# Kernel optimization log

Measured on AMD Instinct MI355X. Metric: run time of the kernel, lower is better.

The kernel has to match this reference:

```python
import jax, jax.numpy as jnp
import numpy as np


def setup_inputs() -> dict:
    key = jax.random.key(0)
    ks = jax.random.split(key, 6)
    B, S, H, F, E = 4, 2048, 1024, 4096, 8
    x = jax.random.normal(ks[0], (B, S, H), dtype=jnp.float32)
    Wr = jax.random.normal(ks[1], (H, E), dtype=jnp.float32) * (1.0 / np.sqrt(H))
    br = jnp.zeros((E,), dtype=jnp.float32)
    W1 = jax.random.normal(ks[2], (E, H, F), dtype=jnp.float32) * (1.0 / np.sqrt(H))
    b1 = jnp.zeros((E, F), dtype=jnp.float32)
    W2 = jax.random.normal(ks[3], (E, F, H), dtype=jnp.float32) * (1.0 / np.sqrt(F))
    b2 = jnp.zeros((E, H), dtype=jnp.float32)
    b_buf = jnp.zeros((E,), dtype=jnp.float32)  # load-balancing bias buffer, zero-init
    return {"x": x, "b_buf": b_buf, "Wr": Wr, "br": br,
            "W1": W1, "b1": b1, "W2": W2, "b2": b2, "k": 2}


def reference(x, b_buf, Wr, br, W1, b1, W2, b2, k):
    # Router
    scores = jnp.einsum('bsh,he->bse', x, Wr) + br          # [B,S,E]
    probs = jax.nn.softmax(scores, axis=-1)
    # load_balancing: expert selection uses biased scores (b_buf pre-update)
    _, expert_id = jax.lax.top_k(probs + b_buf, k)          # [B,S,k] int
    # combine weights use unbiased probs
    p, _ = jax.lax.top_k(probs, k)                          # [B,S,k]
    # Dense-dispatch reference: run every expert MLP on all tokens,
    # then select via one-hot mask (same math as gather/scatter dispatch).
    h1 = jnp.einsum('bsh,ehf->ebsf', x, W1) + b1[:, None, None, :]
    h1 = jax.nn.gelu(h1, approximate=False)                 # torch nn.GELU = exact
    out_e = jnp.einsum('ebsf,efh->ebsh', h1, W2) + b2[:, None, None, :]
    E = W1.shape[0]
    onehot = (expert_id[None, :, :, :] == jnp.arange(E)[:, None, None, None]).astype(x.dtype)  # [E,B,S,k]
    out_k = jnp.einsum('ebsk,ebsh->bskh', onehot, out_e)    # scatter-combine per slot
    w = p / jnp.sum(p, axis=-1, keepdims=True)              # normalize top-k probs
    return jnp.einsum('bsk,bskh->bsh', w, out_k)
```

## Files before the change

### kernel.cpp

```cpp
#include <hip/hip_runtime.h>
#include <stdint.h>

#define NTOK 8192
#define H_ 1024
#define F_ 4096
#define E_ 8
#define ROWS_CAP 17408
#define MBLK 136

using f32x4  = __attribute__((ext_vector_type(4))) float;
using short8 = __attribute__((ext_vector_type(8))) short;

__device__ __forceinline__ ushort f2bf(float f) {
  union { float f; uint32_t u; } v; v.f = f;
  uint32_t r = (v.u + 0x7FFFu + ((v.u >> 16) & 1u)) >> 16;
  return (ushort)r;
}

__global__ void k_init(int* cnt, int* cur, int* tok, float* wl) {
  int i = blockIdx.x * 256 + threadIdx.x;
  if (i < E_) { cnt[i] = 0; cur[i] = 0; }
  if (i < ROWS_CAP) { tok[i] = -1; wl[i] = 0.f; }
}

__global__ __launch_bounds__(256) void k_transcvt(const float* __restrict__ W,
                                                  ushort* __restrict__ WT,
                                                  int R, int C) {
  __shared__ float t[64][65];
  int e = blockIdx.z;
  int c0 = blockIdx.x * 64, r0 = blockIdx.y * 64;
  const float* Wp = W + (size_t)e * R * C;
  ushort* Tp = WT + (size_t)e * R * C;
  int tx = threadIdx.x & 15, ty = threadIdx.x >> 4;
#pragma unroll
  for (int i = 0; i < 4; i++) {
    int lr = ty + i * 16;
    const float4 v = *(const float4*)&Wp[(size_t)(r0 + lr) * C + c0 + tx * 4];
    t[lr][tx * 4 + 0] = v.x; t[lr][tx * 4 + 1] = v.y;
    t[lr][tx * 4 + 2] = v.z; t[lr][tx * 4 + 3] = v.w;
  }
  __syncthreads();
#pragma unroll
  for (int i = 0; i < 4; i++) {
    int lc = ty + i * 16;
    ushort4 o;
    o.x = f2bf(t[tx * 4 + 0][lc]);
    o.y = f2bf(t[tx * 4 + 1][lc]);
    o.z = f2bf(t[tx * 4 + 2][lc]);
    o.w = f2bf(t[tx * 4 + 3][lc]);
    *(ushort4*)&Tp[(size_t)(c0 + lc) * R + r0 + tx * 4] = o;
  }
}

__global__ __launch_bounds__(256) void k_router(const float* __restrict__ x,
                                                const float* __restrict__ Wr,
                                                const float* __restrict__ br,
                                                const float* __restrict__ bbuf,
                                                int* cnt, int* te, float* tw) {
  int wid = threadIdx.x >> 6, lane = threadIdx.x & 63;
  int t = blockIdx.x * 4 + wid;
  const float* xp = x + (size_t)t * H_;
  double acc[E_];
#pragma unroll
  for (int e = 0; e < E_; e++) acc[e] = 0.0;
  for (int j = lane; j < H_; j += 64) {
    float xv = xp[j];
    const float4 w0 = *(const float4*)&Wr[j * 8];
    const float4 w1 = *(const float4*)&Wr[j * 8 + 4];
    acc[0] += (double)xv * (double)w0.x;
    acc[1] += (double)xv * (double)w0.y;
    acc[2] += (double)xv * (double)w0.z;
    acc[3] += (double)xv * (double)w0.w;
    acc[4] += (double)xv * (double)w1.x;
    acc[5] += (double)xv * (double)w1.y;
    acc[6] += (double)xv * (double)w1.z;
    acc[7] += (double)xv * (double)w1.w;
  }
#pragma unroll
  for (int e = 0; e < E_; e++)
    for (int s = 32; s > 0; s >>= 1) acc[e] += __shfl_xor(acc[e], s);
  if (lane == 0) {
    double s[E_], m = -1e300;
    for (int e = 0; e < E_; e++) { s[e] = acc[e] + (double)br[e]; if (s[e] > m) m = s[e]; }
    double pe[E_], sum = 0.0;
    for (int e = 0; e < E_; e++) { pe[e] = exp(s[e] - m); sum += pe[e]; }
    double pr[E_], bb[E_];
    for (int e = 0; e < E_; e++) { pr[e] = pe[e] / sum; bb[e] = pr[e] + (double)bbuf[e]; }
    int e0 = 0;
    for (int e = 1; e < E_; e++) if (bb[e] > bb[e0]) e0 = e;
    int e1 = (e0 == 0) ? 1 : 0;
    for (int e = 0; e < E_; e++) if (e != e0 && bb[e] > bb[e1]) e1 = e;
    int a0 = 0;
    for (int e = 1; e < E_; e++) if (pr[e] > pr[a0]) a0 = e;
    int a1 = (a0 == 0) ? 1 : 0;
    for (int e = 0; e < E_; e++) if (e != a0 && pr[e] > pr[a1]) a1 = e;
    double iv = 1.0 / (pr[a0] + pr[a1]);
    te[t * 2] = e0; te[t * 2 + 1] = e1;
    tw[t * 2] = (float)(pr[a0] * iv); tw[t * 2 + 1] = (float)(pr[a1] * iv);
    atomicAdd(&cnt[e0], 1); atomicAdd(&cnt[e1], 1);
  }
}

__global__ void k_offsets(const int* cnt, int* off) {
  if (threadIdx.x == 0 && blockIdx.x == 0) {
    int o = 0; off[0] = 0;
    for (int e = 0; e < E_; e++) { o += ((cnt[e] + 127) >> 7) << 7; off[e + 1] = o; }
  }
}

__global__ void k_build(const int* __restrict__ te, const float* __restrict__ tw,
                        const int* __restrict__ off, int* cur, int* tok, float* wl) {
  int t = blockIdx.x * 256 + threadIdx.x;
  if (t >= NTOK) return;
#pragma unroll
  for (int s = 0; s < 2; s++) {
    int e = te[t * 2 + s];
    int slot = atomicAdd(&cur[e], 1);
    int pos = off[e] + slot;
    tok[pos] = t; wl[pos] = tw[t * 2 + s];
  }
}

__global__ __launch_bounds__(256) void k_gather(const float* __restrict__ x,
                                                const int* __restrict__ tok,
                                                ushort* __restrict__ Xg) {
  int row = blockIdx.x;
  int t = tok[row];
  if (t < 0) return;
  const float4* src = (const float4*)(x + (size_t)t * H_);
  ushort4* dst = (ushort4*)(Xg + (size_t)row * H_);
  int i = threadIdx.x;
  float4 v = src[i];
  ushort4 o; o.x = f2bf(v.x); o.y = f2bf(v.y); o.z = f2bf(v.z); o.w = f2bf(v.w);
  dst[i] = o;
}

__global__ void k_zero(float* out) {
  size_t i = (size_t)blockIdx.x * 256 + threadIdx.x;
  float4 z; z.x = 0.f; z.y = 0.f; z.z = 0.f; z.w = 0.f;
  ((float4*)out)[i] = z;
}

template <int MODE>
__global__ __launch_bounds__(256) void k_gemm(const ushort* __restrict__ A,
                                              const ushort* __restrict__ BT,
                                              const float* __restrict__ bias,
                                              ushort* __restrict__ Cbf,
                                              float* __restrict__ Out,
                                              const int* __restrict__ off,
                                              const int* __restrict__ tok,
                                              const float* __restrict__ wl,
                                              int K, int N) {
  int row0 = blockIdx.y * 128;
  int lastoff = off[E_];
  if (row0 >= lastoff) return;
  int e = 0;
  while (off[e + 1] <= row0) e++;
  int n0 = blockIdx.x * 128;
  const ushort* Bp = BT + (size_t)e * (size_t)N * (size_t)K;

  __shared__ __align__(16) ushort As[128 * 32];
  __shared__ __align__(16) ushort Bs[128 * 32];

  int tid = threadIdx.x, lane = tid & 63, wid = tid >> 6;
  int wr = wid >> 1, wc = wid & 1;

  f32x4 acc[4][4];
#pragma unroll
  for (int m = 0; m < 4; m++)
#pragma unroll
    for (int n = 0; n < 4; n++) acc[m][n] = (f32x4){0.f, 0.f, 0.f, 0.f};

  int srow = tid >> 1;
  int skh = (tid & 1) * 16;
  const size_t aRowBase = (size_t)(row0 + srow) * (size_t)K + skh;
  const size_t bRowBase = (size_t)(n0 + srow) * (size_t)K + skh;
  int ldsOff = srow * 32 + skh;

  int fr = lane & 15, fq = lane >> 4;
  int aOff0 = (wr * 64 + fr) * 32 + fq * 8;
  int bOff0 = (wc * 64 + fr) * 32 + fq * 8;

  int nk = K >> 5;
  for (int kk = 0; kk < nk; kk++) {
    int k0 = kk << 5;
    uint4 a0 = *(const uint4*)&A[aRowBase + k0];
    uint4 a1 = *(const uint4*)&A[aRowBase + k0 + 8];
    uint4 b0 = *(const uint4*)&Bp[bRowBase + k0];
    uint4 b1 = *(const uint4*)&Bp[bRowBase + k0 + 8];
    __syncthreads();
    *(uint4*)&As[ldsOff] = a0;
    *(uint4*)&As[ldsOff + 8] = a1;
    *(uint4*)&Bs[ldsOff] = b0;
    *(uint4*)&Bs[ldsOff + 8] = b1;
    __syncthreads();
    short8 af[4], bfr[4];
#pragma unroll
    for (int m = 0; m < 4; m++) af[m] = *(const short8*)&As[aOff0 + m * 16 * 32];
#pragma unroll
    for (int n = 0; n < 4; n++) bfr[n] = *(const short8*)&Bs[bOff0 + n * 16 * 32];
#pragma unroll
    for (int m = 0; m < 4; m++)
#pragma unroll
      for (int n = 0; n < 4; n++)
        acc[m][n] = __builtin_amdgcn_mfma_f32_16x16x32_bf16(af[m], bfr[n], acc[m][n], 0, 0, 0);
  }

  const float* bp = bias + (size_t)e * N;
  if (MODE == 0) {
#pragma unroll
    for (int m = 0; m < 4; m++)
#pragma unroll
      for (int n = 0; n < 4; n++)
#pragma unroll
        for (int j = 0; j < 4; j++) {
          int r = row0 + wr * 64 + m * 16 + (fq << 2) + j;
          int c = n0 + wc * 64 + n * 16 + fr;
          float v = acc[m][n][j] + bp[c];
          v = 0.5f * v * (1.0f + erff(v * 0.70710678118654752f));
          Cbf[(size_t)r * (size_t)N + c] = f2bf(v);
        }
  } else {
#pragma unroll
    for (int m = 0; m < 4; m++)
#pragma unroll
      for (int j = 0; j < 4; j++) {
        int r = row0 + wr * 64 + m * 16 + (fq << 2) + j;
        int t = tok[r];
        if (t < 0) continue;
        float w = wl[r];
#pragma unroll
        for (int n = 0; n < 4; n++) {
          int c = n0 + wc * 64 + n * 16 + fr;
          atomicAdd(&Out[(size_t)t * (size_t)N + c], w * (acc[m][n][j] + bp[c]));
        }
      }
  }
}

extern "C" void kernel_launch(void* const* d_in, const int* in_sizes, int n_in,
                              void* d_out, int out_size, void* d_ws, size_t ws_size,
                              hipStream_t stream) {
  (void)in_sizes; (void)n_in; (void)out_size; (void)ws_size;
  const float* x    = (const float*)d_in[0];
  const float* bbuf = (const float*)d_in[1];
  const float* Wr   = (const float*)d_in[2];
  const float* br   = (const float*)d_in[3];
  const float* W1   = (const float*)d_in[4];
  const float* b1   = (const float*)d_in[5];
  const float* W2   = (const float*)d_in[6];
  const float* b2   = (const float*)d_in[7];
  float* out = (float*)d_out;

  char* ws = (char*)d_ws;
  ushort* W1T = (ushort*)ws;
  ushort* W2T = (ushort*)(ws + 67108864);
  ushort* Xg  = (ushort*)(ws + 134217728);
  ushort* h1  = (ushort*)(ws + 169869312);
  char* meta  = ws + 312475648;
  int*   cnt = (int*)(meta);
  int*   off = (int*)(meta + 64);
  int*   cur = (int*)(meta + 128);
  int*   te  = (int*)(meta + 256);
  float* tw  = (float*)(meta + 256 + 65536);
  int*   tok = (int*)(meta + 256 + 131072);
  float* wl  = (float*)(meta + 256 + 131072 + 69632);

  k_init<<<ROWS_CAP / 256, 256, 0, stream>>>(cnt, cur, tok, wl);
  k_transcvt<<<dim3(F_ / 64, H_ / 64, E_), 256, 0, stream>>>(W1, W1T, H_, F_);
  k_transcvt<<<dim3(H_ / 64, F_ / 64, E_), 256, 0, stream>>>(W2, W2T, F_, H_);
  k_router<<<NTOK / 4, 256, 0, stream>>>(x, Wr, br, bbuf, cnt, te, tw);
  k_offsets<<<1, 64, 0, stream>>>(cnt, off);
  k_build<<<NTOK / 256, 256, 0, stream>>>(te, tw, off, cur, tok, wl);
  k_gather<<<ROWS_CAP, 256, 0, stream>>>(x, tok, Xg);
  k_zero<<<(NTOK * H_ / 4) / 256, 256, 0, stream>>>(out);
  k_gemm<0><<<dim3(F_ / 128, MBLK), 256, 0, stream>>>(Xg, W1T, b1, h1, nullptr, off, nullptr, nullptr, H_, F_);
  k_gemm<1><<<dim3(H_ / 128, MBLK), 256, 0, stream>>>(h1, W2T, b2, nullptr, out, off, tok, wl, F_, H_);
}
```

Baseline: 985.3 us.

## Load GEMM tiles directly into LDS and remap blocks for XCD-aware grouped ordering

```diff
diff --git a/kernel.cpp b/kernel.cpp
--- a/kernel.cpp
+++ b/kernel.cpp
@@ -10,6 +10,13 @@
 
 using f32x4  = __attribute__((ext_vector_type(4))) float;
 using short8 = __attribute__((ext_vector_type(8))) short;
+
+typedef __attribute__((address_space(1))) const uint32_t gu32;
+typedef __attribute__((address_space(3))) uint32_t lu32;
+
+__device__ __forceinline__ void glds16(const void* g, void* l) {
+  __builtin_amdgcn_global_load_lds((gu32*)g, (lu32*)l, 16, 0, 0);
+}
 
 __device__ __forceinline__ ushort f2bf(float f) {
   union { float f; uint32_t u; } v; v.f = f;
@@ -150,13 +157,21 @@
                                               const int* __restrict__ off,
                                               const int* __restrict__ tok,
                                               const float* __restrict__ wl,
-                                              int K, int N) {
-  int row0 = blockIdx.y * 128;
+                                              int K, int N, int NT) {
+  int nwg = gridDim.x;
+  int cpx = nwg >> 3;
+  int bid = blockIdx.x;
+  int lid = (bid & 7) * cpx + (bid >> 3);
+  int gsz = NT << 3;
+  int g = lid / gsz, r = lid % gsz;
+  int n = r >> 3;
+  int m = (g << 3) + (r & 7);
+  int row0 = m * 128;
   int lastoff = off[E_];
   if (row0 >= lastoff) return;
   int e = 0;
   while (off[e + 1] <= row0) e++;
-  int n0 = blockIdx.x * 128;
+  int n0 = n * 128;
   const ushort* Bp = BT + (size_t)e * (size_t)N * (size_t)K;
 
   __shared__ __align__(16) ushort As[128 * 32];
@@ -167,72 +182,73 @@
 
   f32x4 acc[4][4];
 #pragma unroll
-  for (int m = 0; m < 4; m++)
-#pragma unroll
-    for (int n = 0; n < 4; n++) acc[m][n] = (f32x4){0.f, 0.f, 0.f, 0.f};
-
-  int srow = tid >> 1;
-  int skh = (tid & 1) * 16;
-  const size_t aRowBase = (size_t)(row0 + srow) * (size_t)K + skh;
-  const size_t bRowBase = (size_t)(n0 + srow) * (size_t)K + skh;
-  int ldsOff = srow * 32 + skh;
+  for (int mm = 0; mm < 4; mm++)
+#pragma unroll
+    for (int nn = 0; nn < 4; nn++) acc[mm][nn] = (f32x4){0.f, 0.f, 0.f, 0.f};
+
+  int srow = (wid << 4) + (lane >> 2);
+  int skb  = (lane & 3) << 4;
+  const char* aG0 = (const char*)(A  + (size_t)(row0 + srow) * K) + skb;
+  const char* aG1 = (const char*)(A  + (size_t)(row0 + 64 + srow) * K) + skb;
+  const char* bG0 = (const char*)(Bp + (size_t)(n0 + srow) * K) + skb;
+  const char* bG1 = (const char*)(Bp + (size_t)(n0 + 64 + srow) * K) + skb;
+  ushort* lA0 = As + (wid << 9);
+  ushort* lA1 = lA0 + 2048;
+  ushort* lB0 = Bs + (wid << 9);
+  ushort* lB1 = lB0 + 2048;
 
   int fr = lane & 15, fq = lane >> 4;
-  int aOff0 = (wr * 64 + fr) * 32 + fq * 8;
-  int bOff0 = (wc * 64 + fr) * 32 + fq * 8;
+  int aOff0 = ((wr << 6) + fr) * 32 + (fq << 3);
+  int bOff0 = ((wc << 6) + fr) * 32 + (fq << 3);
 
   int nk = K >> 5;
   for (int kk = 0; kk < nk; kk++) {
-    int k0 = kk << 5;
-    uint4 a0 = *(const uint4*)&A[aRowBase + k0];
-    uint4 a1 = *(const uint4*)&A[aRowBase + k0 + 8];
-    uint4 b0 = *(const uint4*)&Bp[bRowBase + k0];
-    uint4 b1 = *(const uint4*)&Bp[bRowBase + k0 + 8];
+    size_t kb = (size_t)kk << 6;
     __syncthreads();
-    *(uint4*)&As[ldsOff] = a0;
-    *(uint4*)&As[ldsOff + 8] = a1;
-    *(uint4*)&Bs[ldsOff] = b0;
-    *(uint4*)&Bs[ldsOff + 8] = b1;
+    glds16(aG0 + kb, lA0);
+    glds16(aG1 + kb, lA1);
+    glds16(bG0 + kb, lB0);
+    glds16(bG1 + kb, lB1);
     __syncthreads();
     short8 af[4], bfr[4];
 #pragma unroll
-    for (int m = 0; m < 4; m++) af[m] = *(const short8*)&As[aOff0 + m * 16 * 32];
-#pragma unroll
-    for (int n = 0; n < 4; n++) bfr[n] = *(const short8*)&Bs[bOff0 + n * 16 * 32];
-#pragma unroll
-    for (int m = 0; m < 4; m++)
-#pragma unroll
-      for (int n = 0; n < 4; n++)
-        acc[m][n] = __builtin_amdgcn_mfma_f32_16x16x32_bf16(af[m], bfr[n], acc[m][n], 0, 0, 0);
+    for (int mm = 0; mm < 4; mm++) af[mm] = *(const short8*)&As[aOff0 + mm * 16 * 32];
+#pragma unroll
+    for (int nn = 0; nn < 4; nn++) bfr[nn] = *(const short8*)&Bs[bOff0 + nn * 16 * 32];
+#pragma unroll
+    for (int mm = 0; mm < 4; mm++)
+#pragma unroll
+      for (int nn = 0; nn < 4; nn++)
+        acc[mm][nn] = __builtin_amdgcn_mfma_f32_16x16x32_bf16(af[mm], bfr[nn], acc[mm][nn], 0, 0, 0);
   }
 
   const float* bp = bias + (size_t)e * N;
   if (MODE == 0) {
 #pragma unroll
-    for (int m = 0; m < 4; m++)
-#pragma unroll
-      for (int n = 0; n < 4; n++)
+    for (int mm = 0; mm < 4; mm++)
+#pragma unroll
+      for (int nn = 0; nn < 4; nn++)
 #pragma unroll
         for (int j = 0; j < 4; j++) {
-          int r = row0 + wr * 64 + m * 16 + (fq << 2) + j;
-          int c = n0 + wc * 64 + n * 16 + fr;
-          float v = acc[m][n][j] + bp[c];
+          int rr = row0 + (wr << 6) + mm * 16 + (fq << 2) + j;
+          int c = n0 + (wc << 6) + nn * 16 + fr;
+          float v = acc[mm][nn][j] + bp[c];
           v = 0.5f * v * (1.0f + erff(v * 0.70710678118654752f));
-          Cbf[(size_t)r * (size_t)N + c] = f2bf(v);
+          Cbf[(size_t)rr * (size_t)N + c] = f2bf(v);
         }
   } else {
 #pragma unroll
-    for (int m = 0; m < 4; m++)
+    for (int mm = 0; mm < 4; mm++)
 #pragma unroll
       for (int j = 0; j < 4; j++) {
-        int r = row0 + wr * 64 + m * 16 + (fq << 2) + j;
-        int t = tok[r];
+        int rr = row0 + (wr << 6) + mm * 16 + (fq << 2) + j;
+        int t = tok[rr];
         if (t < 0) continue;
-        float w = wl[r];
-#pragma unroll
-        for (int n = 0; n < 4; n++) {
-          int c = n0 + wc * 64 + n * 16 + fr;
-          atomicAdd(&Out[(size_t)t * (size_t)N + c], w * (acc[m][n][j] + bp[c]));
+        float w = wl[rr];
+#pragma unroll
+        for (int nn = 0; nn < 4; nn++) {
+          int c = n0 + (wc << 6) + nn * 16 + fr;
+          atomicAdd(&Out[(size_t)t * (size_t)N + c], w * (acc[mm][nn][j] + bp[c]));
         }
       }
   }
@@ -274,6 +290,6 @@
   k_build<<<NTOK / 256, 256, 0, stream>>>(te, tw, off, cur, tok, wl);
   k_gather<<<ROWS_CAP, 256, 0, stream>>>(x, tok, Xg);
   k_zero<<<(NTOK * H_ / 4) / 256, 256, 0, stream>>>(out);
-  k_gemm<0><<<dim3(F_ / 128, MBLK), 256, 0, stream>>>(Xg, W1T, b1, h1, nullptr, off, nullptr, nullptr, H_, F_);
-  k_gemm<1><<<dim3(H_ / 128, MBLK), 256, 0, stream>>>(h1, W2T, b2, nullptr, out, off, tok, wl, F_, H_);
-}
+  k_gemm<0><<<32 * MBLK, 256, 0, stream>>>(Xg, W1T, b1, h1, nullptr, off, nullptr, nullptr, H_, F_, 32);
+  k_gemm<1><<<8 * MBLK, 256, 0, stream>>>(h1, W2T, b2, nullptr, out, off, tok, wl, F_, H_, 8);
+}
```

Measured after the change: 934.7 us. 5.1% less time.
